# Kernel optimization log

Hardware: AMD Instinct MI355X
Metric: run time of the kernel (lower is better)

Reference implementation:

```python
import jax, jax.numpy as jnp
import numpy as np

HIDDEN = 2048
HEADS = 16
HEAD_DIM = HIDDEN // HEADS
ROPE_BASE = 10000.0


def apply_rope(x):
    # x: [B, H, S, d]  (Llama-style half-split RoPE)
    d = x.shape[-1]
    S = x.shape[-2]
    inv_freq = 1.0 / (ROPE_BASE ** (jnp.arange(0, d, 2, dtype=jnp.float32) / d))
    freqs = jnp.arange(S, dtype=jnp.float32)[:, None] * inv_freq[None, :]  # [S, d/2]
    cos = jnp.concatenate([jnp.cos(freqs), jnp.cos(freqs)], axis=-1)  # [S, d]
    sin = jnp.concatenate([jnp.sin(freqs), jnp.sin(freqs)], axis=-1)
    x1, x2 = jnp.split(x, 2, axis=-1)
    rot = jnp.concatenate([-x2, x1], axis=-1)
    return x * cos.astype(x.dtype) + rot * sin.astype(x.dtype)


def setup_inputs() -> dict:
    key = jax.random.key(0)
    ks = jax.random.split(key, 6)
    B, S = 4, 1024
    x = jax.random.normal(ks[0], (B, S, HIDDEN), dtype=jnp.float32)
    attention_mask = jnp.zeros((B, S), dtype=jnp.float32)  # additive mask
    scale = 1.0 / np.sqrt(HIDDEN)
    Wq = jax.random.normal(ks[1], (HIDDEN, HIDDEN), dtype=jnp.float32) * scale
    Wk = jax.random.normal(ks[2], (HIDDEN, HIDDEN), dtype=jnp.float32) * scale
    Wv = jax.random.normal(ks[3], (HIDDEN, HIDDEN), dtype=jnp.float32) * scale
    Wo = jax.random.normal(ks[4], (HIDDEN, HIDDEN), dtype=jnp.float32) * scale
    return {"x": x, "attention_mask": attention_mask, "Wq": Wq, "Wk": Wk, "Wv": Wv, "Wo": Wo}


def reference(x, attention_mask, Wq, Wk, Wv, Wo):
    B, S, D = x.shape
    H, d = HEADS, HEAD_DIM
    # projections (nn.Linear: y = x @ W.T, no bias)
    q = jnp.einsum('bsd,ed->bse', x, Wq).reshape(B, S, H, d).transpose(0, 2, 1, 3)
    k = jnp.einsum('bsd,ed->bse', x, Wk).reshape(B, S, H, d).transpose(0, 2, 1, 3)
    v = jnp.einsum('bsd,ed->bse', x, Wv).reshape(B, S, H, d).transpose(0, 2, 1, 3)
    q = apply_rope(q)
    k = apply_rope(k)
    scores = jnp.einsum('bhqd,bhkd->bhqk', q, k) / jnp.sqrt(jnp.float32(d))
    causal = jnp.where(jnp.tril(jnp.ones((S, S), dtype=bool)), 0.0, -jnp.inf).astype(scores.dtype)
    scores = scores + causal[None, None]
    scores = scores + attention_mask[:, None, None, :]
    attn_weights = jax.nn.softmax(scores, axis=-1)
    # dropout is identity in eval mode
    out = jnp.einsum('bhqk,bhkd->bhqd', attn_weights, v)
    out = out.transpose(0, 2, 1, 3).reshape(B, S, D)
    out = jnp.einsum('bsd,ed->bse', out, Wo)
    return (out, attn_weights)
```

## Files before the change

### kernel.cpp

```cpp
#include <hip/hip_runtime.h>
#include <hip/hip_bf16.h>


typedef __attribute__((ext_vector_type(8))) short bf16x8;
typedef __attribute__((ext_vector_type(4))) float f32x4;

#define GLD_LDS16(g, l)                                                      \
  __builtin_amdgcn_global_load_lds(                                          \
      (const __attribute__((address_space(1))) unsigned int*)(g),            \
      (__attribute__((address_space(3))) unsigned int*)(l), 16, 0, 0)

__global__ __launch_bounds__(256) void cast_kernel(
    const float* __restrict__ in, __hip_bfloat16* __restrict__ out, int n8) {
  int idx = blockIdx.x * 256 + threadIdx.x;
  if (idx >= n8) return;
  const float4* p = (const float4*)in;
  float4 a = p[idx * 2], b = p[idx * 2 + 1];
  __hip_bfloat16 h[8] = {__float2bfloat16(a.x), __float2bfloat16(a.y),
                         __float2bfloat16(a.z), __float2bfloat16(a.w),
                         __float2bfloat16(b.x), __float2bfloat16(b.y),
                         __float2bfloat16(b.z), __float2bfloat16(b.w)};
  uint4 u;
  __builtin_memcpy(&u, h, 16);
  ((uint4*)out)[idx] = u;
}

template <int MODE>
__global__ __launch_bounds__(256) void gemm_nt(
    const void* __restrict__ Abase, const __hip_bfloat16* __restrict__ Bbase,
    void* __restrict__ Cbase) {
  __shared__ alignas(16) __hip_bfloat16 lA[128][64];
  __shared__ alignas(16) __hip_bfloat16 lB[128][64];

  const int tid = threadIdx.x;
  const int m0 = blockIdx.y * 128;
  const int n0 = blockIdx.x * 128;
  const int z = blockIdx.z;

  const __hip_bfloat16* A = nullptr;
  const float* A32 = nullptr;
  const __hip_bfloat16* Bm;
  int lda = 2048, ldb = 2048, K = 2048;
  if constexpr (MODE == 0) {
    A = (const __hip_bfloat16*)Abase;
    Bm = Bbase + (size_t)z * (2048 * 2048);
  } else if constexpr (MODE == 1) {
    if (n0 > m0) return;
    int b = z >> 4, h = z & 15;
    A = (const __hip_bfloat16*)Abase + ((size_t)b * 1024) * 2048 + h * 128;
    Bm = Bbase + ((size_t)b * 1024) * 2048 + h * 128;
    K = 128;
  } else if constexpr (MODE == 2) {
    A32 = (const float*)Abase + (size_t)z * (1024 * 1024);
    Bm = Bbase + (size_t)z * (128 * 1024);
    ldb = 1024;
    K = m0 + 128;
  } else {
    A = (const __hip_bfloat16*)Abase;
    Bm = Bbase;
  }

  const int lane = tid & 63;
  const int wid = tid >> 6;
  const int wm = (wid & 1) * 64;
  const int wn = (wid >> 1) * 64;
  const int frow = lane & 15;
  const int fk = (lane >> 4) * 8;

  f32x4 acc[4][4] = {};

  for (int k0 = 0; k0 < K; k0 += 64) {
    __syncthreads();
    if constexpr (MODE == 2) {
#pragma unroll
      for (int c = 0; c < 8; ++c) {
        int lin = c * 256 + tid;
        int r = lin >> 4;
        int col = (lin & 15) << 2;
        float4 v = *(const float4*)&A32[(size_t)(m0 + r) * 1024 + k0 + col];
        __hip_bfloat16 hh[4] = {__float2bfloat16(v.x), __float2bfloat16(v.y),
                                __float2bfloat16(v.z), __float2bfloat16(v.w)};
        unsigned long long u;
        __builtin_memcpy(&u, hh, 8);
        *(unsigned long long*)&lA[r][col] = u;
      }
    } else {
#pragma unroll
      for (int c = 0; c < 4; ++c) {
        int lin = c * 256 + tid;
        int r = lin >> 3;
        int col = (lin & 7) << 3;
        GLD_LDS16(A + (size_t)(m0 + r) * lda + k0 + col, &lA[r][col]);
      }
    }
#pragma unroll
    for (int c = 0; c < 4; ++c) {
      int lin = c * 256 + tid;
      int r = lin >> 3;
      int col = (lin & 7) << 3;
      GLD_LDS16(Bm + (size_t)(n0 + r) * ldb + k0 + col, &lB[r][col]);
    }
    __syncthreads();
#pragma unroll
    for (int kk = 0; kk < 64; kk += 32) {
      bf16x8 av[4], bv[4];
#pragma unroll
      for (int i = 0; i < 4; ++i)
        av[i] = *(const bf16x8*)&lA[wm + i * 16 + frow][kk + fk];
#pragma unroll
      for (int i = 0; i < 4; ++i)
        bv[i] = *(const bf16x8*)&lB[wn + i * 16 + frow][kk + fk];
#pragma unroll
      for (int mi = 0; mi < 4; ++mi)
#pragma unroll
        for (int ni = 0; ni < 4; ++ni)
          acc[mi][ni] = __builtin_amdgcn_mfma_f32_16x16x32_bf16(
              av[mi], bv[ni], acc[mi][ni], 0, 0, 0);
    }
  }

  const int r0 = (lane >> 4) * 4;
  const int cc = lane & 15;

  if constexpr (MODE == 1) {
    float* C = (float*)Cbase + (size_t)z * (1024 * 1024);
    const float scale = 0.08838834764831845f;
#pragma unroll
    for (int mi = 0; mi < 4; ++mi)
#pragma unroll
      for (int ni = 0; ni < 4; ++ni)
#pragma unroll
        for (int r = 0; r < 4; ++r)
          C[(size_t)(m0 + wm + mi * 16 + r0 + r) * 1024 +
            (n0 + wn + ni * 16 + cc)] = acc[mi][ni][r] * scale;
  } else if constexpr (MODE == 3) {
    float* C = (float*)Cbase;
#pragma unroll
    for (int mi = 0; mi < 4; ++mi)
#pragma unroll
      for (int ni = 0; ni < 4; ++ni)
#pragma unroll
        for (int r = 0; r < 4; ++r)
          C[(size_t)(m0 + wm + mi * 16 + r0 + r) * 2048 +
            (n0 + wn + ni * 16 + cc)] = acc[mi][ni][r];
  } else if constexpr (MODE == 0) {
    __hip_bfloat16* C = (__hip_bfloat16*)Cbase + (size_t)z * (4096 * 2048);
#pragma unroll
    for (int mi = 0; mi < 4; ++mi)
#pragma unroll
      for (int ni = 0; ni < 4; ++ni)
#pragma unroll
        for (int r = 0; r < 4; ++r)
          C[(size_t)(m0 + wm + mi * 16 + r0 + r) * 2048 +
            (n0 + wn + ni * 16 + cc)] = __float2bfloat16(acc[mi][ni][r]);
  } else {
    int b = z >> 4, h = z & 15;
    __hip_bfloat16* C =
        (__hip_bfloat16*)Cbase + ((size_t)b * 1024) * 2048 + h * 128;
#pragma unroll
    for (int mi = 0; mi < 4; ++mi)
#pragma unroll
      for (int ni = 0; ni < 4; ++ni)
#pragma unroll
        for (int r = 0; r < 4; ++r)
          C[(size_t)(m0 + wm + mi * 16 + r0 + r) * 2048 +
            (n0 + wn + ni * 16 + cc)] = __float2bfloat16(acc[mi][ni][r]);
  }
}

__global__ __launch_bounds__(256) void rope_kernel(__hip_bfloat16* __restrict__ Qb,
                                                   __hip_bfloat16* __restrict__ Kb) {
  __hip_bfloat16* p = blockIdx.y ? Kb : Qb;
  int idx = blockIdx.x * 256 + threadIdx.x;
  int j = idx & 63;
  int h = (idx >> 6) & 15;
  int spos = (idx >> 10) & 1023;
  int b = idx >> 20;
  float inv_freq = __expf(-((float)(2 * j) / 128.f) * 9.210340371976184f);
  float ang = (float)spos * inv_freq;
  float c = cosf(ang), sn = sinf(ang);
  size_t base = ((size_t)(b * 1024 + spos)) * 2048 + h * 128 + j;
  float x1 = __bfloat162float(p[base]);
  float x2 = __bfloat162float(p[base + 64]);
  p[base] = __float2bfloat16(x1 * c - x2 * sn);
  p[base + 64] = __float2bfloat16(x2 * c + x1 * sn);
}

__global__ __launch_bounds__(256) void transpose_v(
    const __hip_bfloat16* __restrict__ Vb, __hip_bfloat16* __restrict__ Vt) {
  __shared__ __hip_bfloat16 t[64][65];
  int s0 = blockIdx.x * 64;
  int j0 = blockIdx.y * 64;
  int bh = blockIdx.z;
  int b = bh >> 4, h = bh & 15;
  const __hip_bfloat16* src = Vb + ((size_t)b * 1024) * 2048 + h * 128;
#pragma unroll
  for (int it = 0; it < 16; ++it) {
    int lin = it * 256 + threadIdx.x;
    int r = lin >> 6, c = lin & 63;
    t[r][c] = src[(size_t)(s0 + r) * 2048 + j0 + c];
  }
  __syncthreads();
  __hip_bfloat16* dst = Vt + ((size_t)bh * 128 + j0) * 1024 + s0;
#pragma unroll
  for (int it = 0; it < 16; ++it) {
    int lin = it * 256 + threadIdx.x;
    int r = lin >> 6, c = lin & 63;
    dst[(size_t)r * 1024 + c] = t[c][r];
  }
}

__global__ __launch_bounds__(256) void softmax_kernel(
    float* __restrict__ scores, const float* __restrict__ mask) {
  const int row = blockIdx.x;
  const int i = row & 1023;
  const int b = row >> 14;
  float* srow = scores + (size_t)row * 1024;
  const float* mrow = mask + b * 1024;
  const int tid = threadIdx.x;

  float s[4];
  float mx = -3.0e38f;
#pragma unroll
  for (int it = 0; it < 4; ++it) {
    int j = it * 256 + tid;
    float v = -3.0e38f;
    if (j <= i) v = srow[j] + mrow[j];
    s[it] = v;
    mx = fmaxf(mx, v);
  }
#pragma unroll
  for (int off = 32; off > 0; off >>= 1) mx = fmaxf(mx, __shfl_down(mx, off, 64));
  __shared__ float redm[4], reds[4];
  if ((tid & 63) == 0) redm[tid >> 6] = mx;
  __syncthreads();
  mx = fmaxf(fmaxf(redm[0], redm[1]), fmaxf(redm[2], redm[3]));

  float sum = 0.f;
#pragma unroll
  for (int it = 0; it < 4; ++it) {
    float e = (s[it] > -1.0e38f) ? __expf(s[it] - mx) : 0.f;
    s[it] = e;
    sum += e;
  }
#pragma unroll
  for (int off = 32; off > 0; off >>= 1) sum += __shfl_down(sum, off, 64);
  if ((tid & 63) == 0) reds[tid >> 6] = sum;
  __syncthreads();
  sum = reds[0] + reds[1] + reds[2] + reds[3];
  float inv = 1.0f / sum;
#pragma unroll
  for (int it = 0; it < 4; ++it) {
    int j = it * 256 + tid;
    srow[j] = s[it] * inv;
  }
}

extern "C" void kernel_launch(void* const* d_in, const int* in_sizes, int n_in,
                              void* d_out, int out_size, void* d_ws,
                              size_t ws_size, hipStream_t stream) {
  const float* x = (const float*)d_in[0];
  const float* mask = (const float*)d_in[1];
  const float* Wq = (const float*)d_in[2];
  const float* Wk = (const float*)d_in[3];
  const float* Wv = (const float*)d_in[4];
  const float* Wo = (const float*)d_in[5];
  float* out = (float*)d_out;
  float* attnw = out + (size_t)4 * 1024 * 2048;

  __hip_bfloat16* wsb = (__hip_bfloat16*)d_ws;
  __hip_bfloat16* Wob = wsb;
  __hip_bfloat16* xb  = wsb + 4194304;
  __hip_bfloat16* Wqb = wsb + 12582912;
  __hip_bfloat16* Qb  = wsb + 25165824;
  __hip_bfloat16* Kb  = wsb + 33554432;
  __hip_bfloat16* Vb  = wsb + 41943040;
  __hip_bfloat16* Vt  = wsb + 50331648;
  __hip_bfloat16* AO  = wsb + 4194304;

  cast_kernel<<<4096, 256, 0, stream>>>(x, xb, 1048576);
  cast_kernel<<<2048, 256, 0, stream>>>(Wq, Wqb, 524288);
  cast_kernel<<<2048, 256, 0, stream>>>(Wk, Wqb + 4194304, 524288);
  cast_kernel<<<2048, 256, 0, stream>>>(Wv, Wqb + 8388608, 524288);
  cast_kernel<<<2048, 256, 0, stream>>>(Wo, Wob, 524288);

  gemm_nt<0><<<dim3(16, 32, 3), 256, 0, stream>>>(xb, Wqb, Qb);
  rope_kernel<<<dim3(16384, 2), 256, 0, stream>>>(Qb, Kb);
  transpose_v<<<dim3(16, 2, 64), 256, 0, stream>>>(Vb, Vt);
  gemm_nt<1><<<dim3(8, 8, 64), 256, 0, stream>>>(Qb, Kb, attnw);
  softmax_kernel<<<65536, 256, 0, stream>>>(attnw, mask);
  gemm_nt<2><<<dim3(1, 8, 64), 256, 0, stream>>>(attnw, Vt, AO);
  gemm_nt<3><<<dim3(16, 32, 1), 256, 0, stream>>>(AO, Wob, out);
}
```

Baseline: 776.9 us.

## Fuse casts into one kernel, fold RoPE into QKV GEMM epilogue, vectorize transpose/softmax

Merges the five cast launches into a single cast_all kernel. Adds a dedicated QKV GEMM whose 128-wide N tile matches a head, so RoPE is applied in the epilogue and the separate rope pass over Q and K is gone. Vectorizes the V transpose with 16-byte loads and stores, and the softmax with float4 accesses. The new GEMM uses a 32x128 per-wave tile, which changes register pressure and MFMA reuse, and RoPE now uses fast __sincosf.

```diff
diff --git a/kernel.cpp b/kernel.cpp
--- a/kernel.cpp
+++ b/kernel.cpp
@@ -10,19 +10,127 @@
       (const __attribute__((address_space(1))) unsigned int*)(g),            \
       (__attribute__((address_space(3))) unsigned int*)(l), 16, 0, 0)
 
-__global__ __launch_bounds__(256) void cast_kernel(
-    const float* __restrict__ in, __hip_bfloat16* __restrict__ out, int n8) {
+__global__ __launch_bounds__(256) void cast_all(
+    const float* __restrict__ x, const float* __restrict__ Wq,
+    const float* __restrict__ Wk, const float* __restrict__ Wv,
+    const float* __restrict__ Wo, __hip_bfloat16* __restrict__ ws) {
   int idx = blockIdx.x * 256 + threadIdx.x;
-  if (idx >= n8) return;
-  const float4* p = (const float4*)in;
-  float4 a = p[idx * 2], b = p[idx * 2 + 1];
+  const float* src;
+  __hip_bfloat16* dst;
+  int off;
+  if (idx < 1048576) {
+    src = x; dst = ws + 4194304; off = idx;
+  } else if (idx < 1572864) {
+    src = Wq; dst = ws + 12582912; off = idx - 1048576;
+  } else if (idx < 2097152) {
+    src = Wk; dst = ws + 16777216; off = idx - 1572864;
+  } else if (idx < 2621440) {
+    src = Wv; dst = ws + 20971520; off = idx - 2097152;
+  } else {
+    src = Wo; dst = ws; off = idx - 2621440;
+  }
+  const float4* p = (const float4*)src;
+  float4 a = p[(size_t)off * 2], b = p[(size_t)off * 2 + 1];
   __hip_bfloat16 h[8] = {__float2bfloat16(a.x), __float2bfloat16(a.y),
                          __float2bfloat16(a.z), __float2bfloat16(a.w),
                          __float2bfloat16(b.x), __float2bfloat16(b.y),
                          __float2bfloat16(b.z), __float2bfloat16(b.w)};
   uint4 u;
   __builtin_memcpy(&u, h, 16);
-  ((uint4*)out)[idx] = u;
+  ((uint4*)dst)[off] = u;
+}
+
+__global__ __launch_bounds__(256) void gemm_qkv(
+    const __hip_bfloat16* __restrict__ A, const __hip_bfloat16* __restrict__ W,
+    __hip_bfloat16* __restrict__ QKV) {
+  __shared__ alignas(16) __hip_bfloat16 lA[128][64];
+  __shared__ alignas(16) __hip_bfloat16 lB[128][64];
+
+  const int tid = threadIdx.x;
+  const int m0 = blockIdx.y * 128;
+  const int n0 = blockIdx.x * 128;
+  const int z = blockIdx.z;
+  const __hip_bfloat16* Bm = W + (size_t)z * (2048 * 2048);
+
+  const int lane = tid & 63;
+  const int wid = tid >> 6;
+  const int wm = wid * 32;
+  const int frow = lane & 15;
+  const int fk = (lane >> 4) * 8;
+
+  f32x4 acc[2][8] = {};
+
+  for (int k0 = 0; k0 < 2048; k0 += 64) {
+    __syncthreads();
+#pragma unroll
+    for (int c = 0; c < 4; ++c) {
+      int lin = c * 256 + tid;
+      int r = lin >> 3;
+      int col = (lin & 7) << 3;
+      GLD_LDS16(A + (size_t)(m0 + r) * 2048 + k0 + col, &lA[r][col]);
+    }
+#pragma unroll
+    for (int c = 0; c < 4; ++c) {
+      int lin = c * 256 + tid;
+      int r = lin >> 3;
+      int col = (lin & 7) << 3;
+      GLD_LDS16(Bm + (size_t)(n0 + r) * 2048 + k0 + col, &lB[r][col]);
+    }
+    __syncthreads();
+#pragma unroll
+    for (int kk = 0; kk < 64; kk += 32) {
+      bf16x8 av[2], bv[8];
+#pragma unroll
+      for (int i = 0; i < 2; ++i)
+        av[i] = *(const bf16x8*)&lA[wm + i * 16 + frow][kk + fk];
+#pragma unroll
+      for (int i = 0; i < 8; ++i)
+        bv[i] = *(const bf16x8*)&lB[i * 16 + frow][kk + fk];
+#pragma unroll
+      for (int mi = 0; mi < 2; ++mi)
+#pragma unroll
+        for (int ni = 0; ni < 8; ++ni)
+          acc[mi][ni] = __builtin_amdgcn_mfma_f32_16x16x32_bf16(
+              av[mi], bv[ni], acc[mi][ni], 0, 0, 0);
+    }
+  }
+
+  const int r0 = (lane >> 4) * 4;
+  const int cc = lane & 15;
+  __hip_bfloat16* C = QKV + (size_t)z * (4096 * 2048);
+
+  if (z < 2) {
+    float invf[4];
+#pragma unroll
+    for (int ni = 0; ni < 4; ++ni)
+      invf[ni] = __expf(-(float)(ni * 16 + cc) * 0.143911568312128f);
+#pragma unroll
+    for (int mi = 0; mi < 2; ++mi) {
+#pragma unroll
+      for (int rr = 0; rr < 4; ++rr) {
+        int m = m0 + wm + mi * 16 + r0 + rr;
+        float spos = (float)(m & 1023);
+        __hip_bfloat16* crow = C + (size_t)m * 2048 + n0;
+#pragma unroll
+        for (int ni = 0; ni < 4; ++ni) {
+          float sn, c;
+          __sincosf(spos * invf[ni], &sn, &c);
+          float x1 = acc[mi][ni][rr], x2 = acc[mi][ni + 4][rr];
+          crow[ni * 16 + cc] = __float2bfloat16(x1 * c - x2 * sn);
+          crow[(ni + 4) * 16 + cc] = __float2bfloat16(x2 * c + x1 * sn);
+        }
+      }
+    }
+  } else {
+#pragma unroll
+    for (int mi = 0; mi < 2; ++mi)
+#pragma unroll
+      for (int ni = 0; ni < 8; ++ni)
+#pragma unroll
+        for (int rr = 0; rr < 4; ++rr)
+          C[(size_t)(m0 + wm + mi * 16 + r0 + rr) * 2048 +
+            (n0 + ni * 16 + cc)] = __float2bfloat16(acc[mi][ni][rr]);
+  }
 }
 
 template <int MODE>
@@ -41,10 +149,7 @@
   const float* A32 = nullptr;
   const __hip_bfloat16* Bm;
   int lda = 2048, ldb = 2048, K = 2048;
-  if constexpr (MODE == 0) {
-    A = (const __hip_bfloat16*)Abase;
-    Bm = Bbase + (size_t)z * (2048 * 2048);
-  } else if constexpr (MODE == 1) {
+  if constexpr (MODE == 1) {
     if (n0 > m0) return;
     int b = z >> 4, h = z & 15;
     A = (const __hip_bfloat16*)Abase + ((size_t)b * 1024) * 2048 + h * 128;
@@ -143,16 +248,6 @@
         for (int r = 0; r < 4; ++r)
           C[(size_t)(m0 + wm + mi * 16 + r0 + r) * 2048 +
             (n0 + wn + ni * 16 + cc)] = acc[mi][ni][r];
-  } else if constexpr (MODE == 0) {
-    __hip_bfloat16* C = (__hip_bfloat16*)Cbase + (size_t)z * (4096 * 2048);
-#pragma unroll
-    for (int mi = 0; mi < 4; ++mi)
-#pragma unroll
-      for (int ni = 0; ni < 4; ++ni)
-#pragma unroll
-        for (int r = 0; r < 4; ++r)
-          C[(size_t)(m0 + wm + mi * 16 + r0 + r) * 2048 +
-            (n0 + wn + ni * 16 + cc)] = __float2bfloat16(acc[mi][ni][r]);
   } else {
     int b = z >> 4, h = z & 15;
     __hip_bfloat16* C =
@@ -168,45 +263,32 @@
   }
 }
 
-__global__ __launch_bounds__(256) void rope_kernel(__hip_bfloat16* __restrict__ Qb,
-                                                   __hip_bfloat16* __restrict__ Kb) {
-  __hip_bfloat16* p = blockIdx.y ? Kb : Qb;
-  int idx = blockIdx.x * 256 + threadIdx.x;
-  int j = idx & 63;
-  int h = (idx >> 6) & 15;
-  int spos = (idx >> 10) & 1023;
-  int b = idx >> 20;
-  float inv_freq = __expf(-((float)(2 * j) / 128.f) * 9.210340371976184f);
-  float ang = (float)spos * inv_freq;
-  float c = cosf(ang), sn = sinf(ang);
-  size_t base = ((size_t)(b * 1024 + spos)) * 2048 + h * 128 + j;
-  float x1 = __bfloat162float(p[base]);
-  float x2 = __bfloat162float(p[base + 64]);
-  p[base] = __float2bfloat16(x1 * c - x2 * sn);
-  p[base + 64] = __float2bfloat16(x2 * c + x1 * sn);
-}
-
 __global__ __launch_bounds__(256) void transpose_v(
     const __hip_bfloat16* __restrict__ Vb, __hip_bfloat16* __restrict__ Vt) {
-  __shared__ __hip_bfloat16 t[64][65];
+  __shared__ short t[64][65];
   int s0 = blockIdx.x * 64;
   int j0 = blockIdx.y * 64;
   int bh = blockIdx.z;
   int b = bh >> 4, h = bh & 15;
-  const __hip_bfloat16* src = Vb + ((size_t)b * 1024) * 2048 + h * 128;
-#pragma unroll
-  for (int it = 0; it < 16; ++it) {
+  const short* src = (const short*)(Vb + ((size_t)b * 1024) * 2048 + h * 128);
+#pragma unroll
+  for (int it = 0; it < 2; ++it) {
     int lin = it * 256 + threadIdx.x;
-    int r = lin >> 6, c = lin & 63;
-    t[r][c] = src[(size_t)(s0 + r) * 2048 + j0 + c];
+    int r = lin >> 3, c8 = (lin & 7) * 8;
+    bf16x8 v = *(const bf16x8*)&src[(size_t)(s0 + r) * 2048 + j0 + c8];
+#pragma unroll
+    for (int e = 0; e < 8; ++e) t[r][c8 + e] = v[e];
   }
   __syncthreads();
-  __hip_bfloat16* dst = Vt + ((size_t)bh * 128 + j0) * 1024 + s0;
-#pragma unroll
-  for (int it = 0; it < 16; ++it) {
+  short* dst = (short*)(Vt + ((size_t)bh * 128 + j0) * 1024 + s0);
+#pragma unroll
+  for (int it = 0; it < 2; ++it) {
     int lin = it * 256 + threadIdx.x;
-    int r = lin >> 6, c = lin & 63;
-    dst[(size_t)r * 1024 + c] = t[c][r];
+    int r2 = lin >> 3, c8 = (lin & 7) * 8;
+    bf16x8 w;
+#pragma unroll
+    for (int e = 0; e < 8; ++e) w[e] = t[c8 + e][r2];
+    *(bf16x8*)&dst[(size_t)r2 * 1024 + c8] = w;
   }
 }
 
@@ -218,16 +300,16 @@
   float* srow = scores + (size_t)row * 1024;
   const float* mrow = mask + b * 1024;
   const int tid = threadIdx.x;
-
-  float s[4];
+  const int j0 = tid * 4;
+
+  float4 v = *(const float4*)&srow[j0];
+  float4 mk = *(const float4*)&mrow[j0];
+  float s[4] = {v.x + mk.x, v.y + mk.y, v.z + mk.z, v.w + mk.w};
   float mx = -3.0e38f;
 #pragma unroll
-  for (int it = 0; it < 4; ++it) {
-    int j = it * 256 + tid;
-    float v = -3.0e38f;
-    if (j <= i) v = srow[j] + mrow[j];
-    s[it] = v;
-    mx = fmaxf(mx, v);
+  for (int e = 0; e < 4; ++e) {
+    if (j0 + e > i) s[e] = -3.0e38f;
+    mx = fmaxf(mx, s[e]);
   }
 #pragma unroll
   for (int off = 32; off > 0; off >>= 1) mx = fmaxf(mx, __shfl_down(mx, off, 64));
@@ -238,10 +320,10 @@
 
   float sum = 0.f;
 #pragma unroll
-  for (int it = 0; it < 4; ++it) {
-    float e = (s[it] > -1.0e38f) ? __expf(s[it] - mx) : 0.f;
-    s[it] = e;
-    sum += e;
+  for (int e = 0; e < 4; ++e) {
+    float ee = (s[e] > -1.0e38f) ? __expf(s[e] - mx) : 0.f;
+    s[e] = ee;
+    sum += ee;
   }
 #pragma unroll
   for (int off = 32; off > 0; off >>= 1) sum += __shfl_down(sum, off, 64);
@@ -249,11 +331,8 @@
   __syncthreads();
   sum = reds[0] + reds[1] + reds[2] + reds[3];
   float inv = 1.0f / sum;
-#pragma unroll
-  for (int it = 0; it < 4; ++it) {
-    int j = it * 256 + tid;
-    srow[j] = s[it] * inv;
-  }
+  float4 o = {s[0] * inv, s[1] * inv, s[2] * inv, s[3] * inv};
+  *(float4*)&srow[j0] = o;
 }
 
 extern "C" void kernel_launch(void* const* d_in, const int* in_sizes, int n_in,
@@ -277,17 +356,12 @@
   __hip_bfloat16* Vb  = wsb + 41943040;
   __hip_bfloat16* Vt  = wsb + 50331648;
   __hip_bfloat16* AO  = wsb + 4194304;
-
-  cast_kernel<<<4096, 256, 0, stream>>>(x, xb, 1048576);
-  cast_kernel<<<2048, 256, 0, stream>>>(Wq, Wqb, 524288);
-  cast_kernel<<<2048, 256, 0, stream>>>(Wk, Wqb + 4194304, 524288);
-  cast_kernel<<<2048, 256, 0, stream>>>(Wv, Wqb + 8388608, 524288);
-  cast_kernel<<<2048, 256, 0, stream>>>(Wo, Wob, 524288);
-
-  gemm_nt<0><<<dim3(16, 32, 3), 256, 0, stream>>>(xb, Wqb, Qb);
-  rope_kernel<<<dim3(16384, 2), 256, 0, stream>>>(Qb, Kb);
-  transpose_v<<<dim3(16, 2, 64), 256, 0, stream>>>(Vb, Vt);
-  gemm_nt<1><<<dim3(8, 8, 64), 256, 0, stream>>>(Qb, Kb, attnw);
+  (void)Kb; (void)Vb;
+
+  cast_all<<<12288, 256, 0, stream>>>(x, Wq, Wk, Wv, Wo, wsb);
+  gemm_qkv<<<dim3(16, 32, 3), 256, 0, stream>>>(xb, Wqb, Qb);
+  transpose_v<<<dim3(16, 2, 64), 256, 0, stream>>>(wsb + 41943040, Vt);
+  gemm_nt<1><<<dim3(8, 8, 64), 256, 0, stream>>>(Qb, wsb + 33554432, attnw);
   softmax_kernel<<<65536, 256, 0, stream>>>(attnw, mask);
   gemm_nt<2><<<dim3(1, 8, 64), 256, 0, stream>>>(attnw, Vt, AO);
   gemm_nt<3><<<dim3(16, 32, 1), 256, 0, stream>>>(AO, Wob, out);
```

Measured after the change: 734.7 us. -5.4%, faster.
